# Performance work log

Measured on AMD Instinct MI355X. Metric: run time of the kernel, lower is better.

The kernel has to match this reference:

```python
import jax, jax.numpy as jnp
import numpy as np

N_USERS = 10000
RESERVE = 100
N_TOTAL = N_USERS + RESERVE  # 10100 graph nodes (incl. unknown-user slots)
D = 128                      # user_id_embedding_size
B = 2048                     # batch of user ids
AVG_DEG = 32


def _build_friendship_matrix(rng: np.random.Generator) -> np.ndarray:
    # Dense symmetric friendship matrix with 1.0 on the diagonal (self-loop),
    # mirroring torch.diag(ones) + symmetric weighted edge insertion.
    F = np.zeros((N_TOTAL, N_TOTAL), dtype=np.float32)
    np.fill_diagonal(F, 1.0)
    n_edges = N_USERS * AVG_DEG // 2
    src = rng.integers(0, N_USERS, size=n_edges)
    dst = rng.integers(0, N_USERS, size=n_edges)
    w = rng.uniform(0.1, 1.0, size=n_edges).astype(np.float32)
    F[src, dst] = w
    F[dst, src] = w
    return F


def setup_inputs() -> dict:
    key = jax.random.key(0)
    k_ids, k_emb, k_w, k_b = jax.random.split(key, 4)
    rng = np.random.default_rng(0)
    user_ids = jax.random.randint(k_ids, (B,), 0, N_USERS, dtype=jnp.int32)
    friendship_matrix = jnp.asarray(_build_friendship_matrix(rng))      # (N, N)
    # torch init: embeddings ~ U[0,1); Linear weight/bias ~ U[-1/sqrt(d), 1/sqrt(d)]
    user_id_embeddings = jax.random.uniform(k_emb, (N_TOTAL, D), dtype=jnp.float32)
    bound = 1.0 / np.sqrt(D)
    lin_weight = jax.random.uniform(k_w, (D, D), minval=-bound, maxval=bound, dtype=jnp.float32)
    lin_bias = jax.random.uniform(k_b, (D,), minval=-bound, maxval=bound, dtype=jnp.float32)
    return {
        "user_ids": user_ids,
        "friendship_matrix": friendship_matrix,
        "user_id_embeddings": user_id_embeddings,
        "lin_weight": lin_weight,
        "lin_bias": lin_bias,
    }


def reference(user_ids, friendship_matrix, user_id_embeddings, lin_weight, lin_bias):
    # Per user: friends = F[uid]; aggregated = sum_n friends[n] * E[n]
    # Vectorized over the batch: gather rows of F, then one GEMM with E.
    friends = friendship_matrix[user_ids]                 # (B, N)
    aggregated = friends @ user_id_embeddings             # (B, D)
    # torch.nn.Linear: x @ W^T + b
    return aggregated @ lin_weight.T + lin_bias           # (B, D)
```

## Files before the change

### kernel.cpp

```cpp
#include <hip/hip_runtime.h>


#define NTOT 10100
#define NV4  2525
#define DIM  128
#define CAP  256
#define TPB  256
#define NLD  10

__global__ __launch_bounds__(TPB) void friendship_kernel(
    const int*   __restrict__ uids,
    const float* __restrict__ F,
    const float* __restrict__ E,
    const float* __restrict__ W,
    const float* __restrict__ bias,
    float*       __restrict__ out)
{
    __shared__ int   s_idx[CAP];
    __shared__ float s_w[CAP];
    __shared__ int   s_cnt;
    __shared__ float s_red[8][DIM];
    __shared__ float s_agg[DIM];
    __shared__ float s_out[DIM];

    const int row = blockIdx.x;
    const int tid = threadIdx.x;
    const int uid = uids[row];
    const float* Frow = F + (size_t)uid * NTOT;
    const float4* Frow4 = (const float4*)Frow;

    if (tid == 0) s_cnt = 0;
    __syncthreads();

    float4 v[NLD];
    #pragma unroll
    for (int t = 0; t < NLD; ++t) {
        int i  = tid + t * TPB;
        int ic = (i < NV4) ? i : (NV4 - 1);
        v[t] = Frow4[ic];
    }
    #pragma unroll
    for (int t = 0; t < NLD; ++t) {
        int i = tid + t * TPB;
        if (i >= NV4) v[t] = make_float4(0.f, 0.f, 0.f, 0.f);
    }

    #pragma unroll
    for (int t = 0; t < NLD; ++t) {
        int n = (tid + t * TPB) * 4;
        float4 vv = v[t];
        bool ba = vv.x != 0.0f, bb = vv.y != 0.0f, bc = vv.z != 0.0f, bd = vv.w != 0.0f;
        int  m  = (int)ba + (int)bb + (int)bc + (int)bd;
        if (m) {
            int p = atomicAdd(&s_cnt, m);
            if (p + m <= CAP) {
                if (ba) { s_idx[p] = n;     s_w[p] = vv.x; ++p; }
                if (bb) { s_idx[p] = n + 1; s_w[p] = vv.y; ++p; }
                if (bc) { s_idx[p] = n + 2; s_w[p] = vv.z; ++p; }
                if (bd) { s_idx[p] = n + 3; s_w[p] = vv.w; ++p; }
            }
        }
    }
    __syncthreads();

    const int cnt = s_cnt;
    const int g = tid >> 5;
    const int l = tid & 31;

    float4 acc = make_float4(0.f, 0.f, 0.f, 0.f);
    if (cnt <= CAP) {
        int k = g;
        for (; k + 8 < cnt; k += 16) {
            int   n0 = s_idx[k];     float w0 = s_w[k];
            int   n1 = s_idx[k + 8]; float w1 = s_w[k + 8];
            float4 e0 = *(const float4*)(E + (size_t)n0 * DIM + l * 4);
            float4 e1 = *(const float4*)(E + (size_t)n1 * DIM + l * 4);
            acc.x += w0 * e0.x; acc.y += w0 * e0.y; acc.z += w0 * e0.z; acc.w += w0 * e0.w;
            acc.x += w1 * e1.x; acc.y += w1 * e1.y; acc.z += w1 * e1.z; acc.w += w1 * e1.w;
        }
        for (; k < cnt; k += 8) {
            int   n = s_idx[k];
            float w = s_w[k];
            float4 ev = *(const float4*)(E + (size_t)n * DIM + l * 4);
            acc.x += w * ev.x; acc.y += w * ev.y; acc.z += w * ev.z; acc.w += w * ev.w;
        }
    } else {
        for (int n = g; n < NTOT; n += 8) {
            float w = Frow[n];
            float4 ev = *(const float4*)(E + (size_t)n * DIM + l * 4);
            acc.x += w * ev.x; acc.y += w * ev.y; acc.z += w * ev.z; acc.w += w * ev.w;
        }
    }
    *(float4*)&s_red[g][l * 4] = acc;
    __syncthreads();

    if (tid < DIM) {
        float sum = 0.0f;
        #pragma unroll
        for (int gg = 0; gg < 8; ++gg) sum += s_red[gg][tid];
        s_agg[tid] = sum;
    }
    __syncthreads();

    const float4* W4 = (const float4*)W;
    #pragma unroll
    for (int q = 0; q < 16; ++q) {
        int i4 = tid + TPB * q;
        float4 wv = W4[i4];
        int j  = i4 >> 5;
        int dd = (i4 & 31) * 4;
        float4 ag = *(const float4*)&s_agg[dd];
        float p = wv.x * ag.x + wv.y * ag.y + wv.z * ag.z + wv.w * ag.w;
        p += __shfl_xor(p, 16);
        p += __shfl_xor(p, 8);
        p += __shfl_xor(p, 4);
        p += __shfl_xor(p, 2);
        p += __shfl_xor(p, 1);
        if ((tid & 31) == 0) s_out[j] = p;
    }
    __syncthreads();
    if (tid < DIM)
        out[(size_t)row * DIM + tid] = bias[tid] + s_out[tid];
}

extern "C" void kernel_launch(void* const* d_in, const int* in_sizes, int n_in,
                              void* d_out, int out_size, void* d_ws, size_t ws_size,
                              hipStream_t stream) {
    const int*   uids = (const int*)  d_in[0];
    const float* F    = (const float*)d_in[1];
    const float* E    = (const float*)d_in[2];
    const float* W    = (const float*)d_in[3];
    const float* bias = (const float*)d_in[4];
    float*       out  = (float*)d_out;

    const int B = in_sizes[0];
    friendship_kernel<<<B, TPB, 0, stream>>>(uids, F, E, W, bias, out);
}
```

Measured before the change: 30.89 us.

## Process four rows per block with double-buffered prefetch of next friendship row

```diff
diff --git a/kernel.cpp b/kernel.cpp
--- a/kernel.cpp
+++ b/kernel.cpp
@@ -7,6 +7,7 @@
 #define CAP  256
 #define TPB  256
 #define NLD  10
+#define RPB  4
 
 __global__ __launch_bounds__(TPB) void friendship_kernel(
     const int*   __restrict__ uids,
@@ -14,7 +15,8 @@
     const float* __restrict__ E,
     const float* __restrict__ W,
     const float* __restrict__ bias,
-    float*       __restrict__ out)
+    float*       __restrict__ out,
+    int B)
 {
     __shared__ int   s_idx[CAP];
     __shared__ float s_w[CAP];
@@ -23,104 +25,127 @@
     __shared__ float s_agg[DIM];
     __shared__ float s_out[DIM];
 
-    const int row = blockIdx.x;
-    const int tid = threadIdx.x;
-    const int uid = uids[row];
-    const float* Frow = F + (size_t)uid * NTOT;
-    const float4* Frow4 = (const float4*)Frow;
+    const int tid  = threadIdx.x;
+    const int base = blockIdx.x * RPB;
+    const int g = tid >> 5;
+    const int l = tid & 31;
+
+    int uid[RPB];
+    #pragma unroll
+    for (int r = 0; r < RPB; ++r)
+        uid[r] = (base + r < B) ? uids[base + r] : uids[0];
 
     if (tid == 0) s_cnt = 0;
-    __syncthreads();
 
-    float4 v[NLD];
-    #pragma unroll
-    for (int t = 0; t < NLD; ++t) {
-        int i  = tid + t * TPB;
-        int ic = (i < NV4) ? i : (NV4 - 1);
-        v[t] = Frow4[ic];
-    }
-    #pragma unroll
-    for (int t = 0; t < NLD; ++t) {
-        int i = tid + t * TPB;
-        if (i >= NV4) v[t] = make_float4(0.f, 0.f, 0.f, 0.f);
+    float4 bufA[NLD], bufB[NLD];
+    {
+        const float4* Fr4 = (const float4*)(F + (size_t)uid[0] * NTOT);
+        #pragma unroll
+        for (int t = 0; t < NLD; ++t) {
+            int i = tid + t * TPB; int ic = (i < NV4) ? i : (NV4 - 1);
+            bufA[t] = Fr4[ic];
+        }
     }
 
     #pragma unroll
-    for (int t = 0; t < NLD; ++t) {
-        int n = (tid + t * TPB) * 4;
-        float4 vv = v[t];
-        bool ba = vv.x != 0.0f, bb = vv.y != 0.0f, bc = vv.z != 0.0f, bd = vv.w != 0.0f;
-        int  m  = (int)ba + (int)bb + (int)bc + (int)bd;
-        if (m) {
-            int p = atomicAdd(&s_cnt, m);
-            if (p + m <= CAP) {
-                if (ba) { s_idx[p] = n;     s_w[p] = vv.x; ++p; }
-                if (bb) { s_idx[p] = n + 1; s_w[p] = vv.y; ++p; }
-                if (bc) { s_idx[p] = n + 2; s_w[p] = vv.z; ++p; }
-                if (bd) { s_idx[p] = n + 3; s_w[p] = vv.w; ++p; }
+    for (int r = 0; r < RPB; ++r) {
+        if (r + 1 < RPB) {
+            const float4* Fr4 = (const float4*)(F + (size_t)uid[r + 1] * NTOT);
+            if (r & 1) {
+                #pragma unroll
+                for (int t = 0; t < NLD; ++t) {
+                    int i = tid + t * TPB; int ic = (i < NV4) ? i : (NV4 - 1);
+                    bufA[t] = Fr4[ic];
+                }
+            } else {
+                #pragma unroll
+                for (int t = 0; t < NLD; ++t) {
+                    int i = tid + t * TPB; int ic = (i < NV4) ? i : (NV4 - 1);
+                    bufB[t] = Fr4[ic];
+                }
             }
         }
+        __syncthreads();
+
+        #pragma unroll
+        for (int t = 0; t < NLD; ++t) {
+            float4 vv = (r & 1) ? bufB[t] : bufA[t];
+            int i = tid + t * TPB;
+            if (i < NV4) {
+                int n = i * 4;
+                bool ba = vv.x != 0.0f, bb = vv.y != 0.0f, bc = vv.z != 0.0f, bd = vv.w != 0.0f;
+                int  m  = (int)ba + (int)bb + (int)bc + (int)bd;
+                if (m) {
+                    int p = atomicAdd(&s_cnt, m);
+                    if (p + m <= CAP) {
+                        if (ba) { s_idx[p] = n;     s_w[p] = vv.x; ++p; }
+                        if (bb) { s_idx[p] = n + 1; s_w[p] = vv.y; ++p; }
+                        if (bc) { s_idx[p] = n + 2; s_w[p] = vv.z; ++p; }
+                        if (bd) { s_idx[p] = n + 3; s_w[p] = vv.w; ++p; }
+                    }
+                }
+            }
+        }
+        __syncthreads();
+        const int cnt = s_cnt;
+
+        float4 acc = make_float4(0.f, 0.f, 0.f, 0.f);
+        if (cnt <= CAP) {
+            int k = g;
+            for (; k + 8 < cnt; k += 16) {
+                int   n0 = s_idx[k];     float w0 = s_w[k];
+                int   n1 = s_idx[k + 8]; float w1 = s_w[k + 8];
+                float4 e0 = *(const float4*)(E + (size_t)n0 * DIM + l * 4);
+                float4 e1 = *(const float4*)(E + (size_t)n1 * DIM + l * 4);
+                acc.x += w0 * e0.x; acc.y += w0 * e0.y; acc.z += w0 * e0.z; acc.w += w0 * e0.w;
+                acc.x += w1 * e1.x; acc.y += w1 * e1.y; acc.z += w1 * e1.z; acc.w += w1 * e1.w;
+            }
+            for (; k < cnt; k += 8) {
+                int   n = s_idx[k];
+                float w = s_w[k];
+                float4 ev = *(const float4*)(E + (size_t)n * DIM + l * 4);
+                acc.x += w * ev.x; acc.y += w * ev.y; acc.z += w * ev.z; acc.w += w * ev.w;
+            }
+        } else {
+            const float* Frow = F + (size_t)uid[r] * NTOT;
+            for (int n = g; n < NTOT; n += 8) {
+                float w = Frow[n];
+                float4 ev = *(const float4*)(E + (size_t)n * DIM + l * 4);
+                acc.x += w * ev.x; acc.y += w * ev.y; acc.z += w * ev.z; acc.w += w * ev.w;
+            }
+        }
+        *(float4*)&s_red[g][l * 4] = acc;
+        __syncthreads();
+
+        if (tid < DIM) {
+            float sum = 0.0f;
+            #pragma unroll
+            for (int gg = 0; gg < 8; ++gg) sum += s_red[gg][tid];
+            s_agg[tid] = sum;
+        }
+        __syncthreads();
+
+        const float4* W4 = (const float4*)W;
+        #pragma unroll
+        for (int q = 0; q < 16; ++q) {
+            int i4 = tid + TPB * q;
+            float4 wv = W4[i4];
+            int j  = i4 >> 5;
+            int dd = (i4 & 31) * 4;
+            float4 ag = *(const float4*)&s_agg[dd];
+            float p = wv.x * ag.x + wv.y * ag.y + wv.z * ag.z + wv.w * ag.w;
+            p += __shfl_xor(p, 16);
+            p += __shfl_xor(p, 8);
+            p += __shfl_xor(p, 4);
+            p += __shfl_xor(p, 2);
+            p += __shfl_xor(p, 1);
+            if ((tid & 31) == 0) s_out[j] = p;
+        }
+        __syncthreads();
+        if (tid < DIM && base + r < B)
+            out[(size_t)(base + r) * DIM + tid] = bias[tid] + s_out[tid];
+        if (tid == 0) s_cnt = 0;
     }
-    __syncthreads();
-
-    const int cnt = s_cnt;
-    const int g = tid >> 5;
-    const int l = tid & 31;
-
-    float4 acc = make_float4(0.f, 0.f, 0.f, 0.f);
-    if (cnt <= CAP) {
-        int k = g;
-        for (; k + 8 < cnt; k += 16) {
-            int   n0 = s_idx[k];     float w0 = s_w[k];
-            int   n1 = s_idx[k + 8]; float w1 = s_w[k + 8];
-            float4 e0 = *(const float4*)(E + (size_t)n0 * DIM + l * 4);
-            float4 e1 = *(const float4*)(E + (size_t)n1 * DIM + l * 4);
-            acc.x += w0 * e0.x; acc.y += w0 * e0.y; acc.z += w0 * e0.z; acc.w += w0 * e0.w;
-            acc.x += w1 * e1.x; acc.y += w1 * e1.y; acc.z += w1 * e1.z; acc.w += w1 * e1.w;
-        }
-        for (; k < cnt; k += 8) {
-            int   n = s_idx[k];
-            float w = s_w[k];
-            float4 ev = *(const float4*)(E + (size_t)n * DIM + l * 4);
-            acc.x += w * ev.x; acc.y += w * ev.y; acc.z += w * ev.z; acc.w += w * ev.w;
-        }
-    } else {
-        for (int n = g; n < NTOT; n += 8) {
-            float w = Frow[n];
-            float4 ev = *(const float4*)(E + (size_t)n * DIM + l * 4);
-            acc.x += w * ev.x; acc.y += w * ev.y; acc.z += w * ev.z; acc.w += w * ev.w;
-        }
-    }
-    *(float4*)&s_red[g][l * 4] = acc;
-    __syncthreads();
-
-    if (tid < DIM) {
-        float sum = 0.0f;
-        #pragma unroll
-        for (int gg = 0; gg < 8; ++gg) sum += s_red[gg][tid];
-        s_agg[tid] = sum;
-    }
-    __syncthreads();
-
-    const float4* W4 = (const float4*)W;
-    #pragma unroll
-    for (int q = 0; q < 16; ++q) {
-        int i4 = tid + TPB * q;
-        float4 wv = W4[i4];
-        int j  = i4 >> 5;
-        int dd = (i4 & 31) * 4;
-        float4 ag = *(const float4*)&s_agg[dd];
-        float p = wv.x * ag.x + wv.y * ag.y + wv.z * ag.z + wv.w * ag.w;
-        p += __shfl_xor(p, 16);
-        p += __shfl_xor(p, 8);
-        p += __shfl_xor(p, 4);
-        p += __shfl_xor(p, 2);
-        p += __shfl_xor(p, 1);
-        if ((tid & 31) == 0) s_out[j] = p;
-    }
-    __syncthreads();
-    if (tid < DIM)
-        out[(size_t)row * DIM + tid] = bias[tid] + s_out[tid];
 }
 
 extern "C" void kernel_launch(void* const* d_in, const int* in_sizes, int n_in,
@@ -134,5 +159,5 @@
     float*       out  = (float*)d_out;
 
     const int B = in_sizes[0];
-    friendship_kernel<<<B, TPB, 0, stream>>>(uids, F, E, W, bias, out);
+    friendship_kernel<<<(B + RPB - 1) / RPB, TPB, 0, stream>>>(uids, F, E, W, bias, out, B);
 }
```

Measured after the change: 45.08 us. 45.9% more time.
